# Performance work log

Measured on AMD Instinct MI355X. Metric: run time of the kernel, lower is better.

Reference implementation:

```python
import jax, jax.numpy as jnp
import numpy as np

B, N, E, H = 2, 1000, 2000, 128


def setup_inputs() -> dict:
    key = jax.random.key(0)
    k1, k2, k3, k4, k5 = jax.random.split(key, 5)
    node_state = jax.random.normal(k1, (B, N, H), dtype=jnp.float32)
    edge_vec = jax.random.normal(k2, (B, E, H), dtype=jnp.float32)
    node2edge = jax.random.uniform(k3, (B, E, N), dtype=jnp.float32)
    edge2node = jax.random.uniform(k4, (B, N, E), dtype=jnp.float32)
    # xavier_uniform for a (H, H, H) tensor: fan_in = H*H, fan_out = H (torch views last 2 dims)
    bound = float(np.sqrt(6.0 / (H + H * H)))
    edge_network = jax.random.uniform(k5, (H, H, H), dtype=jnp.float32, minval=-bound, maxval=bound)
    return {
        "node_state": node_state,
        "edge_vec": edge_vec,
        "node2edge": node2edge,
        "edge2node": edge2node,
        "edge_network": edge_network,
    }


def reference(node_state, edge_vec, node2edge, edge2node, edge_network):
    # node2edge_emb[b,e,h] = sum_n node2edge[b,e,n] * node_state[b,n,h]
    n2e_emb = jnp.einsum("ben,bnh->beh", node2edge, node_state)
    # per-edge dynamic weight W[b,e,i,j] = sum_h edge_vec[b,e,h] * edge_network[h,i,j],
    # applied to n2e_emb; fused into one contraction (grouped edge-conditioned conv).
    new_n2e = jnp.einsum("beh,hij,bej->bei", edge_vec, edge_network, n2e_emb)
    norm = jnp.sum(edge2node, axis=2, keepdims=True) + 1.0  # [B,N,1]
    agg = (jnp.einsum("bne,bei->bni", edge2node, new_n2e) + node_state) / norm
    return agg
```

## Files before the change

kernel.cpp:

```cpp
#include <hip/hip_runtime.h>
#include <hip/hip_bf16.h>
#include <stdint.h>

#define Bv 2
#define Nv 1000
#define Ev 2000
#define Hv 128

typedef __attribute__((ext_vector_type(8))) short bf16x8;
typedef __attribute__((ext_vector_type(4))) float f32x4;
typedef unsigned short u16;
typedef unsigned int u32;

static __device__ __forceinline__ u32 pack2bf(float a, float b) {
  union { __hip_bfloat162 h; u32 u; } c;
  c.h = __float22bfloat162_rn(make_float2(a, b));
  return c.u;
}
static __device__ __forceinline__ u16 cvt1bf(float a) {
  return (u16)(pack2bf(a, 0.f) & 0xffffu);
}

static __device__ __forceinline__ void gload_lds16(const void* g, void* l) {
  __builtin_amdgcn_global_load_lds(
      (const __attribute__((address_space(1))) void*)g,
      (__attribute__((address_space(3))) void*)l, 16, 0, 0);
}

__global__ void k_prep(const float* __restrict__ en, u16* __restrict__ enbf,
                       const float* __restrict__ ns, u16* __restrict__ nsT) {
  const int bid = blockIdx.x;
  const int t = threadIdx.x;
  if (bid < 1024) {
    size_t idx = ((size_t)bid * 256u + t) * 8u;
    const f32x4* p = (const f32x4*)(en + idx);
    f32x4 a = p[0], b = p[1];
    uint4 o;
    o.x = pack2bf(a.x, a.y);
    o.y = pack2bf(a.z, a.w);
    o.z = pack2bf(b.x, b.y);
    o.w = pack2bf(b.z, b.w);
    *(uint4*)(enbf + idx) = o;
  } else {
    __shared__ float tile[32][33];
    const int zb = bid - 1024;
    const int x = zb & 31, y = (zb >> 5) & 3, z = zb >> 7;
    const float* src = ns + (size_t)z * Nv * Hv;
    u16* dst = nsT + (size_t)z * Hv * 1024;
    const int r0 = x * 32, c0 = y * 32;
    const int tx = t & 31, ty = t >> 5;
#pragma unroll
    for (int rr = 0; rr < 4; ++rr) {
      int r = r0 + ty + rr * 8;
      int c = c0 + tx;
      float v = (r < Nv) ? src[(size_t)r * Hv + c] : 0.f;
      tile[ty + rr * 8][tx] = v;
    }
    __syncthreads();
#pragma unroll
    for (int rr = 0; rr < 4; ++rr) {
      int oc = c0 + ty + rr * 8;
      int orr = r0 + tx;
      dst[(size_t)oc * 1024 + orr] = cvt1bf(tile[tx][ty + rr * 8]);
    }
  }
}

template <int M, int KREAL, int KPAD, int NKC, int KSTEPS, int NMT, bool ROWSUM>
__launch_bounds__(256, 4)
__global__ void k_gemm_flat(const float* __restrict__ A, const u16* __restrict__ BT,
                            float* __restrict__ Cpart, float* __restrict__ nrmpart) {
  __shared__ u16 AL[64 * 136];
  __shared__ float rowsum[64];
  const int id = blockIdx.x;
  const int kcid = id % NKC;
  const int mt = (id / NKC) % NMT;
  const int b = id / (NKC * NMT);
  A     += (size_t)b * M * KREAL;
  BT    += (size_t)b * 128 * KPAD;
  Cpart += (size_t)kcid * (2 * M * 128) + (size_t)b * M * 128;
  if (ROWSUM) nrmpart += (size_t)kcid * (2 * M) + (size_t)b * M;
  const int t = threadIdx.x;
  const int lane = t & 63;
  const int w = t >> 6;
  const int row16 = lane & 15;
  const int kg = lane >> 4;
  const int mrow0 = mt * 64;
  const int mtg = (w >> 1) * 2;
  const int itg = (w & 1) * 4;
  f32x4 acc[2][4];
#pragma unroll
  for (int i = 0; i < 2; ++i)
#pragma unroll
    for (int j = 0; j < 4; ++j) acc[i][j] = (f32x4){0.f, 0.f, 0.f, 0.f};
  if (ROWSUM && t < 64) rowsum[t] = 0.f;

#pragma unroll 1
  for (int s = 0; s < KSTEPS; ++s) {
    const int kc = (kcid * KSTEPS + s) * 128;
    __syncthreads();
#pragma unroll
    for (int r = 0; r < 4; ++r) {
      const int chunk = t + r * 256;
      const int m = chunk >> 4;
      const int jc = (chunk & 15) * 8;
      const int gm = mrow0 + m;
      const int gk = kc + jc;
      f32x4 x0 = {0.f, 0.f, 0.f, 0.f}, x1 = {0.f, 0.f, 0.f, 0.f};
      if (gm < M && gk + 8 <= KREAL) {
        const f32x4* p = (const f32x4*)(A + (size_t)gm * KREAL + gk);
        x0 = p[0];
        x1 = p[1];
      }
      if (ROWSUM) {
        float s8 = x0.x + x0.y + x0.z + x0.w + x1.x + x1.y + x1.z + x1.w;
        s8 += __shfl_down(s8, 8, 16);
        s8 += __shfl_down(s8, 4, 16);
        s8 += __shfl_down(s8, 2, 16);
        s8 += __shfl_down(s8, 1, 16);
        if ((lane & 15) == 0) rowsum[m] += s8;
      }
      uint4 o;
      o.x = pack2bf(x0.x, x0.y);
      o.y = pack2bf(x0.z, x0.w);
      o.z = pack2bf(x1.x, x1.y);
      o.w = pack2bf(x1.z, x1.w);
      *(uint4*)&AL[m * 136 + jc] = o;
    }
    __syncthreads();
#pragma unroll
    for (int kk = 0; kk < 4; ++kk) {
      bf16x8 a[2], bfr[4];
#pragma unroll
      for (int q = 0; q < 2; ++q)
        a[q] = *(const bf16x8*)&AL[((mtg + q) * 16 + row16) * 136 + kk * 32 + kg * 8];
#pragma unroll
      for (int q = 0; q < 4; ++q)
        bfr[q] = *(const bf16x8*)(BT + (size_t)((itg + q) * 16 + row16) * KPAD + kc + kk * 32 + kg * 8);
#pragma unroll
      for (int mi = 0; mi < 2; ++mi)
#pragma unroll
        for (int ii = 0; ii < 4; ++ii)
          acc[mi][ii] = __builtin_amdgcn_mfma_f32_16x16x32_bf16(a[mi], bfr[ii], acc[mi][ii], 0, 0, 0);
    }
  }
  if (ROWSUM && t < 64 && mrow0 + t < M) nrmpart[mrow0 + t] = rowsum[t];
#pragma unroll
  for (int mi = 0; mi < 2; ++mi) {
#pragma unroll
    for (int r = 0; r < 4; ++r) {
      const int lrow = (mtg + mi) * 16 + kg * 4 + r;
      const int gm = mrow0 + lrow;
      if (gm < M) {
#pragma unroll
        for (int ii = 0; ii < 4; ++ii)
          Cpart[(size_t)gm * 128 + (itg + ii) * 16 + row16] = acc[mi][ii][r];
      }
    }
  }
}

__global__ void k_reduce_emb(const float* __restrict__ part, u16* __restrict__ embbf) {
  const int tid = blockIdx.x * 256 + threadIdx.x;
  const size_t e = (size_t)tid * 8;
  const int b = (int)(e / 256000);
  const int rem = (int)(e % 256000);
  const int m = rem >> 7;
  const int j = rem & 127;
  const f32x4* p = (const f32x4*)part + tid * 2;
  f32x4 s0 = {0.f, 0.f, 0.f, 0.f}, s1 = {0.f, 0.f, 0.f, 0.f};
#pragma unroll
  for (int kc = 0; kc < 4; ++kc) {
    s0 += p[(size_t)kc * 128000];
    s1 += p[(size_t)kc * 128000 + 1];
  }
  uint4 o;
  o.x = pack2bf(s0.x, s0.y);
  o.y = pack2bf(s0.z, s0.w);
  o.z = pack2bf(s1.x, s1.y);
  o.w = pack2bf(s1.z, s1.w);
  *(uint4*)(embbf + ((size_t)b * 2048 + m) * 128 + j) = o;
}

__global__ void k_cvt_red(const u16* __restrict__ part2, u16* __restrict__ neweT) {
  const int tid = blockIdx.x * 256 + threadIdx.x;
  const size_t f0 = (size_t)tid * 8;
  const int m0 = (int)(f0 & 2047);
  uint4 o;
  if (m0 >= Ev) {
    o = make_uint4(0, 0, 0, 0);
  } else {
    float s[8] = {0.f, 0.f, 0.f, 0.f, 0.f, 0.f, 0.f, 0.f};
#pragma unroll
    for (int hg = 0; hg < 8; ++hg) {
      uint4 v = *(const uint4*)(part2 + (size_t)hg * 524288 + f0);
      u32 wv[4] = {v.x, v.y, v.z, v.w};
#pragma unroll
      for (int q = 0; q < 4; ++q) {
        s[2 * q]     += __uint_as_float(wv[q] << 16);
        s[2 * q + 1] += __uint_as_float(wv[q] & 0xffff0000u);
      }
    }
    o.x = pack2bf(s[0], s[1]);
    o.y = pack2bf(s[2], s[3]);
    o.z = pack2bf(s[4], s[5]);
    o.w = pack2bf(s[6], s[7]);
  }
  *(uint4*)(neweT + f0) = o;
}

__global__ void k_epi_red(const float* __restrict__ part3, const float* __restrict__ nrmp,
                          const float* __restrict__ ns, float* __restrict__ out) {
  const int tid = blockIdx.x * 256 + threadIdx.x;
  const size_t f0 = (size_t)tid * 4;
  const int row = (int)(f0 >> 7);
  const f32x4* p = (const f32x4*)(part3 + f0);
  f32x4 s = {0.f, 0.f, 0.f, 0.f};
#pragma unroll
  for (int kc = 0; kc < 8; ++kc) s += p[(size_t)kc * 64000];
  float nm = 1.0f;
#pragma unroll
  for (int kc = 0; kc < 8; ++kc) nm += nrmp[(size_t)kc * 2000 + row];
  f32x4 nsv = *(const f32x4*)(ns + f0);
  *(f32x4*)(out + f0) = (s + nsv) * (1.0f / nm);
}

__launch_bounds__(256, 2)
__global__ void k_edge_mix(const float* __restrict__ ev, const u16* __restrict__ embbf,
                           const u16* __restrict__ enbf, u16* __restrict__ part2) {
  __shared__ u16 APL[4][4096];
  __shared__ float EVL[64 * 20];
  const int id = blockIdx.x;
  const int hgrp = id & 7;
  const int rest = id >> 3;
  const int mt = rest & 31;
  const int b = rest >> 5;
  const int h0 = hgrp * 16;
  const int t = threadIdx.x;
  const int lane = t & 63;
  const int w = t >> 6;
  const int row16 = lane & 15;
  const int kg = lane >> 4;
  const int mbase = mt * 64;

  if (t < 64) {
    const int ml = mbase + t;
    const float* src = ev + ((size_t)b * Ev + ml) * Hv + h0;
    const f32x4 z = {0.f, 0.f, 0.f, 0.f};
#pragma unroll
    for (int q = 0; q < 4; ++q) {
      f32x4 v = (ml < Ev) ? *(const f32x4*)(src + q * 4) : z;
      *(f32x4*)&EVL[t * 20 + q * 4] = v;
    }
  }

  bf16x8 bfrag[4][4];
  {
    const u16* ebase = embbf + ((size_t)b * 2048 + mbase) * 128;
#pragma unroll
    for (int mf = 0; mf < 4; ++mf) {
      const u16* rp = ebase + (size_t)(mf * 16 + row16) * 128;
#pragma unroll
      for (int kk = 0; kk < 4; ++kk)
        bfrag[mf][kk] = *(const bf16x8*)(rp + kk * 32 + kg * 8);
    }
  }

  auto STAGE = [&](int h) {
    const char* plane = (const char*)(enbf + (size_t)h * 16384) + (size_t)w * 8192;
    char* dst = (char*)&APL[w][0];
#pragma unroll
    for (int it = 0; it < 8; ++it) {
      const int r = it * 4 + (lane >> 4);
      const int inner = (lane & 15) << 4;
      const int srcb = r * 256 + (inner ^ ((r & 7) << 4));
      gload_lds16(plane + srcb, dst + it * 1024);
    }
  };

  const f32x4 zero4 = {0.f, 0.f, 0.f, 0.f};
  f32x4 pers[2][4];
#pragma unroll
  for (int fi = 0; fi < 2; ++fi)
#pragma unroll
    for (int mf = 0; mf < 4; ++mf) pers[fi][mf] = zero4;

  const int xorv = (row16 & 7) << 4;

  STAGE(h0);
  __syncthreads();

#pragma unroll 1
  for (int hh = 0; hh < 16; ++hh) {
    asm volatile("s_waitcnt vmcnt(0)" ::: "memory");
    __builtin_amdgcn_sched_barrier(0);
    const char* sl = (const char*)&APL[w][0];
    bf16x8 a[2][4];
#pragma unroll
    for (int fi = 0; fi < 2; ++fi) {
      const int rs = fi * 16 + row16;
#pragma unroll
      for (int kk = 0; kk < 4; ++kk)
        a[fi][kk] = *(const bf16x8*)(sl + rs * 256 + ((kk * 64 + kg * 16) ^ xorv));
    }
    if (hh + 1 < 16) {
      asm volatile("s_waitcnt lgkmcnt(0)" ::: "memory");
      __builtin_amdgcn_sched_barrier(0);
      STAGE(h0 + hh + 1);
    }
    f32x4 q[2][4];
#pragma unroll
    for (int fi = 0; fi < 2; ++fi)
#pragma unroll
      for (int mf = 0; mf < 4; ++mf)
        q[fi][mf] = __builtin_amdgcn_mfma_f32_16x16x32_bf16(a[fi][0], bfrag[mf][0], zero4, 0, 0, 0);
#pragma unroll
    for (int kk = 1; kk < 4; ++kk)
#pragma unroll
      for (int fi = 0; fi < 2; ++fi)
#pragma unroll
        for (int mf = 0; mf < 4; ++mf)
          q[fi][mf] = __builtin_amdgcn_mfma_f32_16x16x32_bf16(a[fi][kk], bfrag[mf][kk], q[fi][mf], 0, 0, 0);
    float evv[4];
#pragma unroll
    for (int mf = 0; mf < 4; ++mf)
      evv[mf] = EVL[(mf * 16 + row16) * 20 + hh];
#pragma unroll
    for (int fi = 0; fi < 2; ++fi)
#pragma unroll
      for (int mf = 0; mf < 4; ++mf)
        pers[fi][mf] += evv[mf] * q[fi][mf];
  }

  u16* slice = part2 + (size_t)hgrp * (2 * 128 * 2048);
#pragma unroll
  for (int fi = 0; fi < 2; ++fi) {
#pragma unroll
    for (int mf = 0; mf < 4; ++mf) {
      const int ml = mbase + mf * 16 + row16;
#pragma unroll
      for (int r = 0; r < 4; ++r) {
        const int irow = w * 32 + fi * 16 + kg * 4 + r;
        slice[((size_t)b * 128 + irow) * 2048 + ml] = cvt1bf(pers[fi][mf][r]);
      }
    }
  }
}

extern "C" void kernel_launch(void* const* d_in, const int* in_sizes, int n_in,
                              void* d_out, int out_size, void* d_ws, size_t ws_size,
                              hipStream_t stream) {
  const float* ns  = (const float*)d_in[0];
  const float* ev  = (const float*)d_in[1];
  const float* n2e = (const float*)d_in[2];
  const float* e2n = (const float*)d_in[3];
  const float* en  = (const float*)d_in[4];
  float* out = (float*)d_out;

  char* ws = (char*)d_ws;
  float* part1 = (float*)(ws);
  u16*   part2 = (u16*)  (ws + 8192000);
  float* part3 = (float*)(ws + 16580608);
  float* nrmp  = (float*)(ws + 24772608);
  u16*   embbf = (u16*)  (ws + 24838144);
  u16*   enbf  = (u16*)  (ws + 25886720);
  u16*   nsT   = (u16*)  (ws + 30081024);
  u16*   neweT = (u16*)  (ws + 30605312);

  k_prep<<<dim3(1280), dim3(256), 0, stream>>>(en, enbf, ns, nsT);
  k_gemm_flat<2000, 1000, 1024, 4, 2, 32, false><<<dim3(256), dim3(256), 0, stream>>>(n2e, nsT, part1, nullptr);
  k_reduce_emb<<<dim3(250), dim3(256), 0, stream>>>(part1, embbf);
  k_edge_mix<<<dim3(512), dim3(256), 0, stream>>>(ev, embbf, enbf, part2);
  k_cvt_red<<<dim3(256), dim3(256), 0, stream>>>(part2, neweT);
  k_gemm_flat<1000, 2000, 2048, 8, 2, 16, true><<<dim3(256), dim3(256), 0, stream>>>(e2n, neweT, part3, nrmp);
  k_epi_red<<<dim3(250), dim3(256), 0, stream>>>(part3, nrmp, ns, out);
}
```

Baseline: 62.34 us.

## Fuse emb split-K reduction into edge_mix and move enbf cast into first GEMM

Removes the k_reduce_emb launch. Each k_edge_mix block now sums the four split-K fp32 partials for its 64-row tile, converts them to bf16 in LDS and reads its B fragments from there. The edge_network bf16 conversion moves out of the prep kernel into extra tail blocks of the first GEMM launch, so the prep kernel only transposes node_state. This saves a launch and a round trip through embbf. In exchange, every edge_mix block re-reads the fp32 partials (each is read by 8 h-groups), which adds global traffic and LDS use.

```diff
diff --git a/kernel.cpp b/kernel.cpp
--- a/kernel.cpp
+++ b/kernel.cpp
@@ -27,12 +27,43 @@
       (__attribute__((address_space(3))) void*)l, 16, 0, 0);
 }
 
-__global__ void k_prep(const float* __restrict__ en, u16* __restrict__ enbf,
-                       const float* __restrict__ ns, u16* __restrict__ nsT) {
+__global__ void k_prep_ns(const float* __restrict__ ns, u16* __restrict__ nsT) {
+  __shared__ float tile[32][33];
   const int bid = blockIdx.x;
   const int t = threadIdx.x;
-  if (bid < 1024) {
-    size_t idx = ((size_t)bid * 256u + t) * 8u;
+  const int x = bid & 31, y = (bid >> 5) & 3, z = bid >> 7;
+  const float* src = ns + (size_t)z * Nv * Hv;
+  u16* dst = nsT + (size_t)z * Hv * 1024;
+  const int r0 = x * 32, c0 = y * 32;
+  const int tx = t & 31, ty = t >> 5;
+#pragma unroll
+  for (int rr = 0; rr < 4; ++rr) {
+    int r = r0 + ty + rr * 8;
+    int c = c0 + tx;
+    float v = (r < Nv) ? src[(size_t)r * Hv + c] : 0.f;
+    tile[ty + rr * 8][tx] = v;
+  }
+  __syncthreads();
+#pragma unroll
+  for (int rr = 0; rr < 4; ++rr) {
+    int oc = c0 + ty + rr * 8;
+    int orr = r0 + tx;
+    dst[(size_t)oc * 1024 + orr] = cvt1bf(tile[tx][ty + rr * 8]);
+  }
+}
+
+template <int M, int KREAL, int KPAD, int NKC, int KSTEPS, int NMT, bool ROWSUM, bool FCVT>
+__launch_bounds__(256, 4)
+__global__ void k_gemm_flat(const float* __restrict__ A, const u16* __restrict__ BT,
+                            float* __restrict__ Cpart, float* __restrict__ nrmpart,
+                            const float* __restrict__ en, u16* __restrict__ enbf) {
+  __shared__ u16 AL[64 * 136];
+  __shared__ float rowsum[64];
+  const int id = blockIdx.x;
+  const int t = threadIdx.x;
+  if (FCVT && id >= NKC * NMT * 2) {
+    const int cb = id - NKC * NMT * 2;
+    size_t idx = ((size_t)cb * 256u + t) * 8u;
     const f32x4* p = (const f32x4*)(en + idx);
     f32x4 a = p[0], b = p[1];
     uint4 o;
@@ -41,38 +72,8 @@
     o.z = pack2bf(b.x, b.y);
     o.w = pack2bf(b.z, b.w);
     *(uint4*)(enbf + idx) = o;
-  } else {
-    __shared__ float tile[32][33];
-    const int zb = bid - 1024;
-    const int x = zb & 31, y = (zb >> 5) & 3, z = zb >> 7;
-    const float* src = ns + (size_t)z * Nv * Hv;
-    u16* dst = nsT + (size_t)z * Hv * 1024;
-    const int r0 = x * 32, c0 = y * 32;
-    const int tx = t & 31, ty = t >> 5;
-#pragma unroll
-    for (int rr = 0; rr < 4; ++rr) {
-      int r = r0 + ty + rr * 8;
-      int c = c0 + tx;
-      float v = (r < Nv) ? src[(size_t)r * Hv + c] : 0.f;
-      tile[ty + rr * 8][tx] = v;
-    }
-    __syncthreads();
-#pragma unroll
-    for (int rr = 0; rr < 4; ++rr) {
-      int oc = c0 + ty + rr * 8;
-      int orr = r0 + tx;
-      dst[(size_t)oc * 1024 + orr] = cvt1bf(tile[tx][ty + rr * 8]);
-    }
-  }
-}
-
-template <int M, int KREAL, int KPAD, int NKC, int KSTEPS, int NMT, bool ROWSUM>
-__launch_bounds__(256, 4)
-__global__ void k_gemm_flat(const float* __restrict__ A, const u16* __restrict__ BT,
-                            float* __restrict__ Cpart, float* __restrict__ nrmpart) {
-  __shared__ u16 AL[64 * 136];
-  __shared__ float rowsum[64];
-  const int id = blockIdx.x;
+    return;
+  }
   const int kcid = id % NKC;
   const int mt = (id / NKC) % NMT;
   const int b = id / (NKC * NMT);
@@ -80,7 +81,6 @@
   BT    += (size_t)b * 128 * KPAD;
   Cpart += (size_t)kcid * (2 * M * 128) + (size_t)b * M * 128;
   if (ROWSUM) nrmpart += (size_t)kcid * (2 * M) + (size_t)b * M;
-  const int t = threadIdx.x;
   const int lane = t & 63;
   const int w = t >> 6;
   const int row16 = lane & 15;
@@ -160,28 +160,6 @@
   }
 }
 
-__global__ void k_reduce_emb(const float* __restrict__ part, u16* __restrict__ embbf) {
-  const int tid = blockIdx.x * 256 + threadIdx.x;
-  const size_t e = (size_t)tid * 8;
-  const int b = (int)(e / 256000);
-  const int rem = (int)(e % 256000);
-  const int m = rem >> 7;
-  const int j = rem & 127;
-  const f32x4* p = (const f32x4*)part + tid * 2;
-  f32x4 s0 = {0.f, 0.f, 0.f, 0.f}, s1 = {0.f, 0.f, 0.f, 0.f};
-#pragma unroll
-  for (int kc = 0; kc < 4; ++kc) {
-    s0 += p[(size_t)kc * 128000];
-    s1 += p[(size_t)kc * 128000 + 1];
-  }
-  uint4 o;
-  o.x = pack2bf(s0.x, s0.y);
-  o.y = pack2bf(s0.z, s0.w);
-  o.z = pack2bf(s1.x, s1.y);
-  o.w = pack2bf(s1.z, s1.w);
-  *(uint4*)(embbf + ((size_t)b * 2048 + m) * 128 + j) = o;
-}
-
 __global__ void k_cvt_red(const u16* __restrict__ part2, u16* __restrict__ neweT) {
   const int tid = blockIdx.x * 256 + threadIdx.x;
   const size_t f0 = (size_t)tid * 8;
@@ -226,9 +204,10 @@
 }
 
 __launch_bounds__(256, 2)
-__global__ void k_edge_mix(const float* __restrict__ ev, const u16* __restrict__ embbf,
+__global__ void k_edge_mix(const float* __restrict__ ev, const float* __restrict__ part1,
                            const u16* __restrict__ enbf, u16* __restrict__ part2) {
   __shared__ u16 APL[4][4096];
+  __shared__ u16 U[64 * 136];
   __shared__ float EVL[64 * 20];
   const int id = blockIdx.x;
   const int hgrp = id & 7;
@@ -243,6 +222,24 @@
   const int kg = lane >> 4;
   const int mbase = mt * 64;
 
+  {
+    const float* pb = part1 + (size_t)b * 256000 + (size_t)mbase * 128;
+#pragma unroll
+    for (int r = 0; r < 8; ++r) {
+      const int chunk = t + r * 256;
+      const int row = chunk >> 5;
+      const int c4 = (chunk & 31) * 4;
+      const int gm = mbase + row;
+      f32x4 s = {0.f, 0.f, 0.f, 0.f};
+      if (gm < Ev) {
+        const float* p = pb + (size_t)row * 128 + c4;
+#pragma unroll
+        for (int kc = 0; kc < 4; ++kc) s += *(const f32x4*)(p + (size_t)kc * 512000);
+      }
+      *(uint2*)&U[row * 136 + c4] = make_uint2(pack2bf(s.x, s.y), pack2bf(s.z, s.w));
+    }
+  }
+
   if (t < 64) {
     const int ml = mbase + t;
     const float* src = ev + ((size_t)b * Ev + ml) * Hv + h0;
@@ -251,18 +248,6 @@
     for (int q = 0; q < 4; ++q) {
       f32x4 v = (ml < Ev) ? *(const f32x4*)(src + q * 4) : z;
       *(f32x4*)&EVL[t * 20 + q * 4] = v;
-    }
-  }
-
-  bf16x8 bfrag[4][4];
-  {
-    const u16* ebase = embbf + ((size_t)b * 2048 + mbase) * 128;
-#pragma unroll
-    for (int mf = 0; mf < 4; ++mf) {
-      const u16* rp = ebase + (size_t)(mf * 16 + row16) * 128;
-#pragma unroll
-      for (int kk = 0; kk < 4; ++kk)
-        bfrag[mf][kk] = *(const bf16x8*)(rp + kk * 32 + kg * 8);
     }
   }
 
@@ -278,6 +263,16 @@
     }
   };
 
+  STAGE(h0);
+  __syncthreads();
+
+  bf16x8 bfrag[4][4];
+#pragma unroll
+  for (int mf = 0; mf < 4; ++mf)
+#pragma unroll
+    for (int kk = 0; kk < 4; ++kk)
+      bfrag[mf][kk] = *(const bf16x8*)&U[(mf * 16 + row16) * 136 + kk * 32 + kg * 8];
+
   const f32x4 zero4 = {0.f, 0.f, 0.f, 0.f};
   f32x4 pers[2][4];
 #pragma unroll
@@ -286,9 +281,6 @@
     for (int mf = 0; mf < 4; ++mf) pers[fi][mf] = zero4;
 
   const int xorv = (row16 & 7) << 4;
-
-  STAGE(h0);
-  __syncthreads();
 
 #pragma unroll 1
   for (int hh = 0; hh < 16; ++hh) {
@@ -362,16 +354,16 @@
   u16*   part2 = (u16*)  (ws + 8192000);
   float* part3 = (float*)(ws + 16580608);
   float* nrmp  = (float*)(ws + 24772608);
-  u16*   embbf = (u16*)  (ws + 24838144);
-  u16*   enbf  = (u16*)  (ws + 25886720);
-  u16*   nsT   = (u16*)  (ws + 30081024);
-  u16*   neweT = (u16*)  (ws + 30605312);
-
-  k_prep<<<dim3(1280), dim3(256), 0, stream>>>(en, enbf, ns, nsT);
-  k_gemm_flat<2000, 1000, 1024, 4, 2, 32, false><<<dim3(256), dim3(256), 0, stream>>>(n2e, nsT, part1, nullptr);
-  k_reduce_emb<<<dim3(250), dim3(256), 0, stream>>>(part1, embbf);
-  k_edge_mix<<<dim3(512), dim3(256), 0, stream>>>(ev, embbf, enbf, part2);
+  u16*   enbf  = (u16*)  (ws + 24838144);
+  u16*   nsT   = (u16*)  (ws + 29032448);
+  u16*   neweT = (u16*)  (ws + 29556736);
+
+  k_prep_ns<<<dim3(256), dim3(256), 0, stream>>>(ns, nsT);
+  k_gemm_flat<2000, 1000, 1024, 4, 2, 32, false, true>
+      <<<dim3(1280), dim3(256), 0, stream>>>(n2e, nsT, part1, nullptr, en, enbf);
+  k_edge_mix<<<dim3(512), dim3(256), 0, stream>>>(ev, part1, enbf, part2);
   k_cvt_red<<<dim3(256), dim3(256), 0, stream>>>(part2, neweT);
-  k_gemm_flat<1000, 2000, 2048, 8, 2, 16, true><<<dim3(256), dim3(256), 0, stream>>>(e2n, neweT, part3, nrmp);
+  k_gemm_flat<1000, 2000, 2048, 8, 2, 16, true, false>
+      <<<dim3(256), dim3(256), 0, stream>>>(e2n, neweT, part3, nrmp, nullptr, nullptr);
   k_epi_red<<<dim3(250), dim3(256), 0, stream>>>(part3, nrmp, ns, out);
 }
```

After: 65.22 us. 1.05x slower.
